# Optimization experiments

Hardware: AMD Instinct MI355X
Metric: run time of the kernel (lower is better)

## Reference

```python
import jax, jax.numpy as jnp
import numpy as np

B, T, C, H = 4, 2048, 1024, 16
HD = C // H  # head_dim = 64


def _rope(x, cos, sin):
    # x: [B,H,T,HD]; cos/sin: [T,HD//2] -> broadcast [1,1,T,HD//2]
    x1 = x[..., 0::2]
    x2 = x[..., 1::2]
    cos = cos[None, None]
    sin = sin[None, None]
    o1 = x1 * cos - x2 * sin
    o2 = x1 * sin + x2 * cos
    # interleave back to [..., HD]
    return jnp.stack([o1, o2], axis=-1).reshape(x.shape)


def setup_inputs() -> dict:
    key = jax.random.key(0)
    ks = jax.random.split(key, 10)
    x = jax.random.normal(ks[0], (B, T, C), jnp.float32)
    # rotary frequencies (llama-style, theta=10000), stored as (cos,sin)
    inv_freq = 1.0 / (10000.0 ** (jnp.arange(0, HD, 2, dtype=jnp.float32) / HD))
    freqs = jnp.outer(jnp.arange(T, dtype=jnp.float32), inv_freq)  # [T, HD/2]
    freqs_cis = jnp.stack([jnp.cos(freqs), jnp.sin(freqs)], axis=-1)  # [T, HD/2, 2]
    attn_mask = jnp.tril(jnp.ones((T, T), jnp.int32))  # causal
    padding_mask = jnp.ones((B, T), jnp.int32)
    w = 0.02
    Wq = jax.random.normal(ks[1], (C, C), jnp.float32) * w
    Wk = jax.random.normal(ks[2], (C, C), jnp.float32) * w
    Wv = jax.random.normal(ks[3], (C, C), jnp.float32) * w
    Wp = jax.random.normal(ks[4], (C, C), jnp.float32) * w
    bq = jnp.zeros((C,), jnp.float32)
    bk = jnp.zeros((C,), jnp.float32)
    bv = jnp.zeros((C,), jnp.float32)
    bp = jnp.zeros((C,), jnp.float32)
    return {"x": x, "freqs_cis": freqs_cis, "attn_mask": attn_mask,
            "padding_mask": padding_mask, "Wq": Wq, "bq": bq, "Wk": Wk,
            "bk": bk, "Wv": Wv, "bv": bv, "Wp": Wp, "bp": bp}


def reference(x, freqs_cis, attn_mask, padding_mask, Wq, bq, Wk, bk, Wv, bv, Wp, bp):
    b, t, c = x.shape
    # qkv projections -> [B,H,T,HD]
    def heads(y):
        return y.reshape(b, t, H, HD).transpose(0, 2, 1, 3)
    q = heads(x @ Wq.T + bq)
    k = heads(x @ Wk.T + bk)
    v = heads(x @ Wv.T + bv)
    cos, sin = freqs_cis[..., 0], freqs_cis[..., 1]  # [T, HD/2]
    q = _rope(q, cos, sin)
    k = _rope(k, cos, sin)
    att = jnp.einsum('bhqd,bhkd->bhqk', q, k) * (1.0 / np.sqrt(HD).astype(np.float32))
    att = jnp.where(attn_mask[None, None] == 0, -1e30, att)
    att = jnp.where(padding_mask[:, None, None, :] == 0, -1e30, att)
    att = jax.nn.softmax(att, axis=-1)
    # dropout omitted (eval mode / deterministic reference)
    y = jnp.einsum('bhqk,bhkd->bhqd', att, v)
    y = y.transpose(0, 2, 1, 3).reshape(b, t, c)
    return y @ Wp.T + bp
```

## Files before the change

### kernel.cpp

```cpp
#include <hip/hip_runtime.h>
#include <hip/hip_bf16.h>

#define TB 2048
#define CC 1024
#define NH 16
#define HD 64
#define NB 4
#define BHX (NB*NH)
#define BTX (NB*TB)

typedef __attribute__((ext_vector_type(8))) short bf16x8;
typedef __attribute__((ext_vector_type(4))) float f32x4;
typedef __attribute__((ext_vector_type(4))) unsigned short us4;

__device__ __forceinline__ unsigned short bfb(float f) {
  __hip_bfloat16 h = __float2bfloat16(f);
  return __builtin_bit_cast(unsigned short, h);
}
__device__ __forceinline__ float fexp2(float x) {
  return __builtin_amdgcn_exp2f(x);
}
template <int CTRL>
__device__ __forceinline__ float dppf(float x) {
  int r = __builtin_amdgcn_update_dpp(0, __builtin_bit_cast(int, x), CTRL, 0xf, 0xf, false);
  return __builtin_bit_cast(float, r);
}

__device__ __forceinline__ void gld_lds16(const void* g, void* l) {
  __builtin_amdgcn_global_load_lds(
      (const __attribute__((address_space(1))) unsigned*)g,
      (__attribute__((address_space(3))) unsigned*)l, 16, 0, 0);
}

__global__ void cvt_f32_bf16(const float* __restrict__ src,
                             unsigned short* __restrict__ dst, int n4) {
  int i = blockIdx.x * blockDim.x + threadIdx.x;
  if (i >= n4) return;
  f32x4 v = ((const f32x4*)src)[i];
  us4 o;
#pragma unroll
  for (int j = 0; j < 4; j++) o[j] = bfb(v[j]);
  ((us4*)dst)[i] = o;
}

__global__ void cvt_w4(const float* __restrict__ s0, const float* __restrict__ s1,
                       const float* __restrict__ s2, const float* __restrict__ s3,
                       unsigned short* __restrict__ d0, unsigned short* __restrict__ d1,
                       unsigned short* __restrict__ d2, unsigned short* __restrict__ d3) {
  int y = blockIdx.y;
  const float* s = y == 0 ? s0 : y == 1 ? s1 : y == 2 ? s2 : s3;
  unsigned short* d = y == 0 ? d0 : y == 1 ? d1 : y == 2 ? d2 : d3;
  int i = blockIdx.x * 256 + threadIdx.x;
  f32x4 v = ((const f32x4*)s)[i];
  us4 o;
#pragma unroll
  for (int j = 0; j < 4; j++) o[j] = bfb(v[j]);
  ((us4*)d)[i] = o;
}

__global__ void prep_bias(const float* __restrict__ bq, const float* __restrict__ bk,
                          const float* __restrict__ bv, float* __restrict__ out) {
  int i = blockIdx.x * 256 + threadIdx.x;
  float v = i < 1024 ? bq[i] : i < 2048 ? bk[i - 1024] : bv[i - 2048];
  out[i] = v;
}

template <int MODE>
__global__ __launch_bounds__(256) void gemm_bt(
    const unsigned short* __restrict__ A, const unsigned short* __restrict__ Bw,
    const float* __restrict__ bias, const float* __restrict__ fcg,
    void* __restrict__ Cout, int M, int N, int K, int nbx)
{
  __shared__ __align__(16) unsigned short As[2][4096];
  __shared__ __align__(16) unsigned short Bs[2][4096];
  int tid = threadIdx.x;
  int lane = tid & 63, wid = tid >> 6;
  int g = lane >> 4, l4 = lane & 15;
  int wr = wid >> 1, wc = wid & 1;
  const int cpx = gridDim.x >> 3;
  const int swz = (blockIdx.x & 7) * cpx + (blockIdx.x >> 3);
  const int bx = swz % nbx, by = swz / nbx;
  const int brow = by * 128, bcol = bx * 128;

  const unsigned short* ap = A + (size_t)(brow + (tid >> 2)) * K + (tid & 3) * 8;
  const unsigned short* bp_ = Bw + (size_t)(bcol + (tid >> 2)) * K + (tid & 3) * 8;
  const size_t rstep = (size_t)64 * K;
  const int lo = tid * 8;

  f32x4 acc[4][4] = {};

  gld_lds16(ap,          &As[0][lo]);
  gld_lds16(ap + rstep,  &As[0][lo + 2048]);
  gld_lds16(bp_,         &Bs[0][lo]);
  gld_lds16(bp_ + rstep, &Bs[0][lo + 2048]);
  ap += 32; bp_ += 32;
  __syncthreads();

  const int nk = K >> 5;
  for (int kk = 0; kk < nk; kk++) {
    const int cur = kk & 1;
    if (kk + 1 < nk) {
      gld_lds16(ap,          &As[cur ^ 1][lo]);
      gld_lds16(ap + rstep,  &As[cur ^ 1][lo + 2048]);
      gld_lds16(bp_,         &Bs[cur ^ 1][lo]);
      gld_lds16(bp_ + rstep, &Bs[cur ^ 1][lo + 2048]);
      ap += 32; bp_ += 32;
    }
    bf16x8 af[4], bfr[4];
#pragma unroll
    for (int i = 0; i < 4; i++)
      af[i] = *(const bf16x8*)&As[cur][(wr * 64 + i * 16 + l4) * 32 + g * 8];
#pragma unroll
    for (int i = 0; i < 4; i++)
      bfr[i] = *(const bf16x8*)&Bs[cur][(wc * 64 + i * 16 + l4) * 32 + g * 8];
    __builtin_amdgcn_s_setprio(1);
#pragma unroll
    for (int i = 0; i < 4; i++)
#pragma unroll
      for (int j = 0; j < 4; j++)
        acc[i][j] = __builtin_amdgcn_mfma_f32_16x16x32_bf16(af[i], bfr[j], acc[i][j], 0, 0, 0);
    __builtin_amdgcn_s_setprio(0);
    __syncthreads();
  }

#pragma unroll
  for (int i = 0; i < 4; i++) {
    int grow0 = brow + wr * 64 + i * 16 + 4 * g;
#pragma unroll
    for (int j = 0; j < 4; j++) {
      int gcol = bcol + wc * 64 + j * 16 + l4;
      float bv = bias[gcol];
      if (MODE == 0) {
        float* out = (float*)Cout;
#pragma unroll
        for (int r = 0; r < 4; r++)
          out[(size_t)(grow0 + r) * N + gcol] = acc[i][j][r] + bv;
      } else {
        unsigned short* out = (unsigned short*)Cout;
        int part = gcol >> 10;
        int c = gcol & 1023;
        int h = c >> 6, d = c & 63;
        int dbase = d & ~1;
        float sgn = (d & 1) ? 1.f : -1.f;
        bool isqk = (part < 2);
#pragma unroll
        for (int r = 0; r < 4; r++) {
          int grow = grow0 + r;
          int b = grow >> 11, t = grow & 2047;
          float v = acc[i][j][r] + bv;
          float w = __shfl_xor(v, 1, 64);
          float o = v;
          if (isqk) {
            float cth = fcg[(size_t)t * 64 + dbase];
            float sth = fcg[(size_t)t * 64 + dbase + 1];
            o = v * cth + sgn * w * sth;
          }
          size_t dst = (size_t)part * ((size_t)BHX * TB * HD)
                     + ((size_t)(b * NH + h) * TB + t) * HD + d;
          out[dst] = bfb(o);
        }
      }
    }
  }
}

__global__ void transpose_v(const unsigned short* __restrict__ v,
                            unsigned short* __restrict__ vT) {
  int bh = blockIdx.y, t0 = blockIdx.x * 64;
  __shared__ __align__(16) unsigned short tile[64][72];
  int tid = threadIdx.x;
#pragma unroll
  for (int s = 0; s < 2; s++) {
    int cid = tid + 256 * s;
    int r = cid >> 3, c8 = (cid & 7) * 8;
    bf16x8 val = *(const bf16x8*)(v + ((size_t)bh * TB + t0 + r) * HD + c8);
    *(bf16x8*)&tile[r][c8] = val;
  }
  __syncthreads();
#pragma unroll
  for (int s = 0; s < 2; s++) {
    int cid = tid + 256 * s;
    int rr = cid >> 3, cc = (cid & 7) * 8;
    bf16x8 o;
#pragma unroll
    for (int i = 0; i < 8; i++) o[i] = (short)tile[cc + i][rr];
    *(bf16x8*)(vT + ((size_t)bh * HD + rr) * TB + t0 + cc) = o;
  }
}

__global__ __launch_bounds__(256, 4) void flash_fwd(
    const unsigned short* __restrict__ q, const unsigned short* __restrict__ k,
    const unsigned short* __restrict__ vT, unsigned short* __restrict__ yb)
{
  __shared__ __align__(16) unsigned short Ks[2][4096];
  __shared__ __align__(16) unsigned short Vs[2][4096];
  __shared__ __align__(16) unsigned short Ps[4][16][64];

  const int tid = threadIdx.x, wid = tid >> 6, lane = tid & 63;
  const int g = lane >> 4, l4 = lane & 15;

  const int b = blockIdx.x;
  const int xcd = b & 7;
  const int idx = b >> 3;
  const int bh = (xcd << 3) | (idx & 7);
  const int p = idx >> 3;

  const int off0 = tid << 4;
  const int row0 = off0 >> 7, sc0 = ((off0 >> 4) & 7) ^ (row0 & 7);
  const int off1 = off0 + 4096;
  const int row1 = off1 >> 7, sc1 = ((off1 >> 4) & 7) ^ (row1 & 7);
  const int koff0 = (row0 << 6) + (sc0 << 3);
  const int koff1 = (row1 << 6) + (sc1 << 3);
  const int voff0 = (row0 << 11) + (sc0 << 3);
  const int voff1 = (row1 << 11) + (sc1 << 3);

  const float SCL2 = 0.18033688011112042f;

  const unsigned short* kb = k  + ((size_t)bh << 17);
  const unsigned short* vb = vT + ((size_t)bh << 17);

#pragma unroll 1
  for (int sel = 0; sel < 2; sel++) {
    const int q64 = sel ? (31 - p) : p;
    const int rbase = q64 * 64 + wid * 16;

    bf16x8 qf0, qf1;
    {
      const unsigned short* qp = q + (((size_t)bh * TB + rbase + l4) << 6);
      qf0 = *(const bf16x8*)(qp + g * 8);
      qf1 = *(const bf16x8*)(qp + 32 + g * 8);
    }

    float m_run[4], l_run[4];
    f32x4 acc_o[4] = {};
#pragma unroll
    for (int j = 0; j < 4; j++) { m_run[j] = -1e30f; l_run[j] = 0.f; }

    gld_lds16(kb + koff0, &Ks[0][off0 >> 1]);
    gld_lds16(kb + koff1, &Ks[0][off1 >> 1]);
    gld_lds16(vb + voff0, &Vs[0][off0 >> 1]);
    gld_lds16(vb + voff1, &Vs[0][off1 >> 1]);
    __syncthreads();

    for (int kt = 0; kt <= q64; kt++) {
      const int cur = kt & 1;
      if (kt < q64) {
        const int kadd = (kt + 1) << 12;
        const int vadd = (kt + 1) << 6;
        gld_lds16(kb + koff0 + kadd, &Ks[cur ^ 1][off0 >> 1]);
        gld_lds16(kb + koff1 + kadd, &Ks[cur ^ 1][off1 >> 1]);
        gld_lds16(vb + voff0 + vadd, &Vs[cur ^ 1][off0 >> 1]);
        gld_lds16(vb + voff1 + vadd, &Vs[cur ^ 1][off1 >> 1]);
      }
      const unsigned short* Kc = Ks[cur];
      const unsigned short* Vc = Vs[cur];

      float sv[4][4];
      __builtin_amdgcn_s_setprio(1);
#pragma unroll
      for (int cb = 0; cb < 4; cb++) {
        const int r = cb * 16 + l4;
        const int sw = (r & 7) * 8;
        bf16x8 kb0 = *(const bf16x8*)&Kc[r * 64 + ((g * 8) ^ sw)];
        bf16x8 kb1 = *(const bf16x8*)&Kc[r * 64 + (((g + 4) * 8) ^ sw)];
        f32x4 z = {0.f, 0.f, 0.f, 0.f};
        z = __builtin_amdgcn_mfma_f32_16x16x32_bf16(qf0, kb0, z, 0, 0, 0);
        z = __builtin_amdgcn_mfma_f32_16x16x32_bf16(qf1, kb1, z, 0, 0, 0);
#pragma unroll
        for (int j = 0; j < 4; j++)
          sv[cb][j] = z[j] * SCL2;
      }
      __builtin_amdgcn_s_setprio(0);
      if (kt == q64) {
        const int rq = wid * 16 + 4 * g;
#pragma unroll
        for (int cb = 0; cb < 4; cb++)
#pragma unroll
          for (int j = 0; j < 4; j++)
            if (cb * 16 + l4 > rq + j) sv[cb][j] = -1e30f;
      }

      float mt[4];
#pragma unroll
      for (int j = 0; j < 4; j++) {
        float m = fmaxf(fmaxf(sv[0][j], sv[1][j]), fmaxf(sv[2][j], sv[3][j]));
        m = fmaxf(m, dppf<0x121>(m));
        m = fmaxf(m, dppf<0x122>(m));
        m = fmaxf(m, dppf<0x124>(m));
        m = fmaxf(m, dppf<0x128>(m));
        mt[j] = m;
      }
      bool need = !((mt[0] <= m_run[0] + 8.f) & (mt[1] <= m_run[1] + 8.f) &
                    (mt[2] <= m_run[2] + 8.f) & (mt[3] <= m_run[3] + 8.f));
      if (__any(need)) {
#pragma unroll
        for (int j = 0; j < 4; j++) {
          float mn = fmaxf(m_run[j], mt[j]);
          float alpha = fexp2(m_run[j] - mn);
          m_run[j] = mn;
          l_run[j] *= alpha;
#pragma unroll
          for (int db = 0; db < 4; db++) acc_o[db][j] *= alpha;
        }
      }
#pragma unroll
      for (int j = 0; j < 4; j++) {
        float s0 = fexp2(sv[0][j] - m_run[j]); sv[0][j] = s0;
        float s1 = fexp2(sv[1][j] - m_run[j]); sv[1][j] = s1;
        float s2 = fexp2(sv[2][j] - m_run[j]); sv[2][j] = s2;
        float s3 = fexp2(sv[3][j] - m_run[j]); sv[3][j] = s3;
        float p2 = (s0 + s1) + (s2 + s3);
        p2 += dppf<0x121>(p2);
        p2 += dppf<0x122>(p2);
        p2 += dppf<0x124>(p2);
        p2 += dppf<0x128>(p2);
        l_run[j] += p2;
      }

#pragma unroll
      for (int cb = 0; cb < 4; cb++)
#pragma unroll
        for (int j = 0; j < 4; j++) {
          const int xch = (cb * 2 + (l4 >> 3)) ^ ((g & 1) * 4 + j);
          Ps[wid][4 * g + j][xch * 8 + (l4 & 7)] = bfb(sv[cb][j]);
        }
      asm volatile("s_waitcnt lgkmcnt(0)" ::: "memory");
      __builtin_amdgcn_sched_barrier(0);
      bf16x8 pa0 = *(const bf16x8*)&Ps[wid][l4][(g ^ (l4 & 7)) * 8];
      bf16x8 pa1 = *(const bf16x8*)&Ps[wid][l4][((4 + g) ^ (l4 & 7)) * 8];
      __builtin_amdgcn_s_setprio(1);
#pragma unroll
      for (int db = 0; db < 4; db++) {
        const int r = db * 16 + l4;
        const int sw = (r & 7) * 8;
        bf16x8 vb0 = *(const bf16x8*)&Vc[r * 64 + ((g * 8) ^ sw)];
        bf16x8 vb1 = *(const bf16x8*)&Vc[r * 64 + (((g + 4) * 8) ^ sw)];
        acc_o[db] = __builtin_amdgcn_mfma_f32_16x16x32_bf16(pa0, vb0, acc_o[db], 0, 0, 0);
        acc_o[db] = __builtin_amdgcn_mfma_f32_16x16x32_bf16(pa1, vb1, acc_o[db], 0, 0, 0);
      }
      __builtin_amdgcn_s_setprio(0);
      __syncthreads();
    }

    unsigned short* yp = yb + ((size_t)(bh >> 4) * TB) * CC + (size_t)(bh & 15) * HD;
    const int qr0 = rbase + 4 * g;
    float inv[4];
#pragma unroll
    for (int j = 0; j < 4; j++) inv[j] = 1.0f / l_run[j];
#pragma unroll
    for (int db = 0; db < 4; db++) {
      const int d = db * 16 + l4;
#pragma unroll
      for (int j = 0; j < 4; j++)
        yp[(size_t)(qr0 + j) * CC + d] = bfb(acc_o[db][j] * inv[j]);
    }
  }
}

extern "C" void kernel_launch(void* const* d_in, const int* in_sizes, int n_in,
                              void* d_out, int out_size, void* d_ws, size_t ws_size,
                              hipStream_t stream) {
  (void)in_sizes; (void)n_in; (void)out_size; (void)ws_size;
  const float* x  = (const float*)d_in[0];
  const float* fc = (const float*)d_in[1];
  const float* Wq = (const float*)d_in[4];
  const float* bq = (const float*)d_in[5];
  const float* Wk = (const float*)d_in[6];
  const float* bk = (const float*)d_in[7];
  const float* Wv = (const float*)d_in[8];
  const float* bv = (const float*)d_in[9];
  const float* Wp = (const float*)d_in[10];
  const float* bp = (const float*)d_in[11];

  char* ws = (char*)d_ws;
  unsigned short* xb   = (unsigned short*)(ws + 0);
  unsigned short* wqkv = (unsigned short*)(ws + 16777216);
  unsigned short* wp   = (unsigned short*)(ws + 23068672);
  float*          bqkv = (float*)(ws + 25165824);
  unsigned short* qkv  = (unsigned short*)(ws + 25182208);
  unsigned short* vT   = qkv + 3 * (size_t)8388608;
  unsigned short* yb   = xb;

  cvt_f32_bf16<<<(2097152 + 255) / 256, 256, 0, stream>>>(x, xb, 2097152);
  cvt_w4<<<dim3(1024, 4), 256, 0, stream>>>(Wq, Wk, Wv, Wp,
      wqkv, wqkv + 1048576, wqkv + 2097152, wp);
  prep_bias<<<dim3(12), 256, 0, stream>>>(bq, bk, bv, bqkv);

  gemm_bt<1><<<dim3(1536), 256, 0, stream>>>(xb, wqkv, bqkv, fc, qkv, BTX, 3072, 1024, 24);
  transpose_v<<<dim3(32, 64), 256, 0, stream>>>(qkv + 2 * (size_t)8388608, vT);
  flash_fwd<<<dim3(1024), 256, 0, stream>>>(qkv, qkv + (size_t)8388608, vT, yb);
  gemm_bt<0><<<dim3(512), 256, 0, stream>>>(yb, wp, bp, nullptr, (float*)d_out, BTX, 1024, 1024, 8);
}
```

Baseline: 221.7 us.

## Split QKV GEMM into dedicated 256x128-tile kernel with swizzled LDS layout

Replaces the templated GEMM with two specialized kernels. The QKV projection now uses a 256x128 block tile (8x4 MFMA fragments per wave), which halves the grid and raises operand reuse per LDS load. It also adds an XOR swizzle on the LDS column chunks to reduce bank conflicts. The projection GEMM keeps the old 128x128 tile with compile-time constants. The trade-off is more accumulator registers (128 floats per thread), which may lower occupancy or cause spills.

```diff
diff --git a/kernel.cpp b/kernel.cpp
--- a/kernel.cpp
+++ b/kernel.cpp
@@ -65,21 +65,126 @@
   out[i] = v;
 }
 
-template <int MODE>
-__global__ __launch_bounds__(256) void gemm_bt(
+__global__ __launch_bounds__(256) void gemm_qkv(
     const unsigned short* __restrict__ A, const unsigned short* __restrict__ Bw,
     const float* __restrict__ bias, const float* __restrict__ fcg,
-    void* __restrict__ Cout, int M, int N, int K, int nbx)
+    unsigned short* __restrict__ Cout)
 {
+  const int K = 1024, N = 3072;
+  __shared__ __align__(16) unsigned short As[2][256 * 32];
+  __shared__ __align__(16) unsigned short Bs[2][128 * 32];
+  const int tid = threadIdx.x;
+  const int lane = tid & 63, wid = tid >> 6;
+  const int g = lane >> 4, l4 = lane & 15;
+  const int wr = wid >> 1, wc = wid & 1;
+  const int swz = (blockIdx.x & 7) * 96 + (blockIdx.x >> 3);
+  const int bx = swz % 24, by = swz / 24;
+  const int brow = by * 256, bcol = bx * 128;
+
+  int arow[4], acsc[4];
+#pragma unroll
+  for (int s = 0; s < 4; s++) {
+    int c = tid + 256 * s;
+    arow[s] = c >> 2;
+    acsc[s] = (c & 3) ^ (arow[s] & 3);
+  }
+  int brow_[2], bcsc[2];
+#pragma unroll
+  for (int s = 0; s < 2; s++) {
+    int c = tid + 256 * s;
+    brow_[s] = c >> 2;
+    bcsc[s] = (c & 3) ^ (brow_[s] & 3);
+  }
+
+  f32x4 acc[8][4] = {};
+
+#pragma unroll
+  for (int s = 0; s < 4; s++)
+    gld_lds16(A + (size_t)(brow + arow[s]) * K + acsc[s] * 8, &As[0][(tid + 256 * s) * 8]);
+#pragma unroll
+  for (int s = 0; s < 2; s++)
+    gld_lds16(Bw + (size_t)(bcol + brow_[s]) * K + bcsc[s] * 8, &Bs[0][(tid + 256 * s) * 8]);
+  __syncthreads();
+
+  const int nk = K >> 5;
+  for (int kk = 0; kk < nk; kk++) {
+    const int cur = kk & 1;
+    if (kk + 1 < nk) {
+      const int k0 = (kk + 1) << 5;
+#pragma unroll
+      for (int s = 0; s < 4; s++)
+        gld_lds16(A + (size_t)(brow + arow[s]) * K + k0 + acsc[s] * 8, &As[cur ^ 1][(tid + 256 * s) * 8]);
+#pragma unroll
+      for (int s = 0; s < 2; s++)
+        gld_lds16(Bw + (size_t)(bcol + brow_[s]) * K + k0 + bcsc[s] * 8, &Bs[cur ^ 1][(tid + 256 * s) * 8]);
+    }
+    bf16x8 af[8], bfr[4];
+#pragma unroll
+    for (int mf = 0; mf < 8; mf++) {
+      const int r = wr * 128 + mf * 16 + l4;
+      af[mf] = *(const bf16x8*)&As[cur][r * 32 + ((g * 8) ^ ((r & 3) * 8))];
+    }
+#pragma unroll
+    for (int nf = 0; nf < 4; nf++) {
+      const int r = wc * 64 + nf * 16 + l4;
+      bfr[nf] = *(const bf16x8*)&Bs[cur][r * 32 + ((g * 8) ^ ((r & 3) * 8))];
+    }
+    __builtin_amdgcn_s_setprio(1);
+#pragma unroll
+    for (int mf = 0; mf < 8; mf++)
+#pragma unroll
+      for (int nf = 0; nf < 4; nf++)
+        acc[mf][nf] = __builtin_amdgcn_mfma_f32_16x16x32_bf16(af[mf], bfr[nf], acc[mf][nf], 0, 0, 0);
+    __builtin_amdgcn_s_setprio(0);
+    __syncthreads();
+  }
+
+#pragma unroll
+  for (int mf = 0; mf < 8; mf++) {
+    const int grow0 = brow + wr * 128 + mf * 16 + 4 * g;
+#pragma unroll
+    for (int nf = 0; nf < 4; nf++) {
+      const int gcol = bcol + wc * 64 + nf * 16 + l4;
+      const float bv = bias[gcol];
+      const int part = gcol >> 10;
+      const int c = gcol & 1023;
+      const int h = c >> 6, d = c & 63;
+      const int dbase = d & ~1;
+      const float sgn = (d & 1) ? 1.f : -1.f;
+      const bool isqk = (part < 2);
+#pragma unroll
+      for (int r = 0; r < 4; r++) {
+        const int grow = grow0 + r;
+        const int b = grow >> 11, t = grow & 2047;
+        float v = acc[mf][nf][r] + bv;
+        float w = __shfl_xor(v, 1, 64);
+        float o = v;
+        if (isqk) {
+          float cth = fcg[(size_t)t * 64 + dbase];
+          float sth = fcg[(size_t)t * 64 + dbase + 1];
+          o = v * cth + sgn * w * sth;
+        }
+        size_t dst = (size_t)part * ((size_t)BHX * TB * HD)
+                   + ((size_t)(b * NH + h) * TB + t) * HD + d;
+        Cout[dst] = bfb(o);
+      }
+    }
+  }
+}
+
+__global__ __launch_bounds__(256) void gemm_proj(
+    const unsigned short* __restrict__ A, const unsigned short* __restrict__ Bw,
+    const float* __restrict__ bias, float* __restrict__ Cout)
+{
+  const int K = 1024, N = 1024;
   __shared__ __align__(16) unsigned short As[2][4096];
   __shared__ __align__(16) unsigned short Bs[2][4096];
   int tid = threadIdx.x;
   int lane = tid & 63, wid = tid >> 6;
   int g = lane >> 4, l4 = lane & 15;
   int wr = wid >> 1, wc = wid & 1;
-  const int cpx = gridDim.x >> 3;
-  const int swz = (blockIdx.x & 7) * cpx + (blockIdx.x >> 3);
-  const int bx = swz % nbx, by = swz / nbx;
+  const int swz = (blockIdx.x & 7) * 64 + (blockIdx.x >> 3);
+  const int bx = swz % 8, by = swz / 8;
   const int brow = by * 128, bcol = bx * 128;
 
   const unsigned short* ap = A + (size_t)(brow + (tid >> 2)) * K + (tid & 3) * 8;
@@ -130,36 +235,9 @@
     for (int j = 0; j < 4; j++) {
       int gcol = bcol + wc * 64 + j * 16 + l4;
       float bv = bias[gcol];
-      if (MODE == 0) {
-        float* out = (float*)Cout;
-#pragma unroll
-        for (int r = 0; r < 4; r++)
-          out[(size_t)(grow0 + r) * N + gcol] = acc[i][j][r] + bv;
-      } else {
-        unsigned short* out = (unsigned short*)Cout;
-        int part = gcol >> 10;
-        int c = gcol & 1023;
-        int h = c >> 6, d = c & 63;
-        int dbase = d & ~1;
-        float sgn = (d & 1) ? 1.f : -1.f;
-        bool isqk = (part < 2);
-#pragma unroll
-        for (int r = 0; r < 4; r++) {
-          int grow = grow0 + r;
-          int b = grow >> 11, t = grow & 2047;
-          float v = acc[i][j][r] + bv;
-          float w = __shfl_xor(v, 1, 64);
-          float o = v;
-          if (isqk) {
-            float cth = fcg[(size_t)t * 64 + dbase];
-            float sth = fcg[(size_t)t * 64 + dbase + 1];
-            o = v * cth + sgn * w * sth;
-          }
-          size_t dst = (size_t)part * ((size_t)BHX * TB * HD)
-                     + ((size_t)(b * NH + h) * TB + t) * HD + d;
-          out[dst] = bfb(o);
-        }
-      }
+#pragma unroll
+      for (int r = 0; r < 4; r++)
+        Cout[(size_t)(grow0 + r) * N + gcol] = acc[i][j][r] + bv;
     }
   }
 }
@@ -386,8 +464,8 @@
       wqkv, wqkv + 1048576, wqkv + 2097152, wp);
   prep_bias<<<dim3(12), 256, 0, stream>>>(bq, bk, bv, bqkv);
 
-  gemm_bt<1><<<dim3(1536), 256, 0, stream>>>(xb, wqkv, bqkv, fc, qkv, BTX, 3072, 1024, 24);
+  gemm_qkv<<<dim3(768), 256, 0, stream>>>(xb, wqkv, bqkv, fc, qkv);
   transpose_v<<<dim3(32, 64), 256, 0, stream>>>(qkv + 2 * (size_t)8388608, vT);
   flash_fwd<<<dim3(1024), 256, 0, stream>>>(qkv, qkv + (size_t)8388608, vT, yb);
-  gemm_bt<0><<<dim3(512), 256, 0, stream>>>(yb, wp, bp, nullptr, (float*)d_out, BTX, 1024, 1024, 8);
-}
+  gemm_proj<<<dim3(512), 256, 0, stream>>>(yb, wp, bp, (float*)d_out);
+}
```

Result: slower. 260.2 us (+17.4%).
